# Optimization experiments

Measured on AMD Instinct MI355X. Metric: run time of the kernel, lower is better.

The kernel has to match this reference:

```python
import itertools
import jax, jax.numpy as jnp
import numpy as np

N, C, D, S = 512, 128, 16, 10  # atoms, channels, irreps dim (0e+1o+2e+3o), species
IR_DIMS = {'0e': 1, '1o': 3}
MULS = {'0e': (23, 4, 1), '1o': (33, 6, 1)}  # path multiplicities for orders (3, 2, 1)


def _make_u(key, order, mul, ir_dim):
    # Synthetic stand-in for e3nn.reduced_symmetric_tensor_product_basis:
    # under permutation of the `order` leading D axes.
    shape = (D,) * order + (mul, ir_dim)
    u = jax.random.normal(key, shape, dtype=jnp.float32)
    mask = jax.random.bernoulli(jax.random.fold_in(key, 1), 0.1, shape)
    u = jnp.where(mask, u, 0.0)
    perms = list(itertools.permutations(range(order)))
    u = sum(jnp.transpose(u, p + (order, order + 1)) for p in perms) / len(perms)
    return u


def setup_inputs() -> dict:
    key = jax.random.key(0)
    ks = jax.random.split(key, 16)
    inp = {
        'x': jax.random.normal(ks[0], (N, C, D), dtype=jnp.float32),
        'index': jax.random.randint(ks[1], (N,), 0, S, dtype=jnp.int32),
    }
    i = 2
    for ir in IR_DIMS:
        for order, mul in zip((3, 2, 1), MULS[ir]):
            inp[f'u{order}_{ir}'] = _make_u(ks[i], order, mul, IR_DIMS[ir]); i += 1
            # gradient_normalization='element' -> init stddev mul**-0.5, no runtime scale
            inp[f'w{order}_{ir}'] = (jax.random.normal(ks[i], (S, mul, C), dtype=jnp.float32)
                                     * mul ** -0.5); i += 1
    return inp


def _contract(x, idx, u3, u2, u1, w3, w2, w1):
    # x: (N,C,D); uK: (D,)*K + (mulK, ir); wK: (S, mulK, C)
    w3i, w2i, w1i = w3[idx], w2[idx], w1[idx]  # species gather -> (N, mulK, C)
    # order 3: einsum('...jki,kc,cj->c...i', u3, w3i, x) batched over atoms.
    # Form p[n,c,k,j] = w3i[n,k,c]*x[n,c,j] first (small), then one big contraction.
    p = jnp.einsum('nkc,ncj->nckj', w3i, x)              # (N,C,mul3,D)
    out = jnp.einsum('abjki,nckj->ncabi', u3, p)         # (N,C,D,D,ir)
    # order 2: accumulate U2.w2, then contract one D axis with x
    out = out + jnp.einsum('abki,nkc->ncabi', u2, w2i)   # (N,C,D,D,ir)
    out = jnp.einsum('ncaji,ncj->ncai', out, x)          # (N,C,D,ir)
    # order 1: accumulate U1.w1, then final contraction with x
    out = out + jnp.einsum('aki,nkc->ncai', u1, w1i)     # (N,C,D,ir)
    out = jnp.einsum('ncji,ncj->nci', out, x)            # (N,C,ir)
    return out


def reference(x, index, u3_0e, w3_0e, u2_0e, w2_0e, u1_0e, w1_0e,
              u3_1o, w3_1o, u2_1o, w2_1o, u1_1o, w1_1o):
    out0 = _contract(x, index, u3_0e, u2_0e, u1_0e, w3_0e, w2_0e, w1_0e)  # (N,C,1)
    out1 = _contract(x, index, u3_1o, u2_1o, u1_1o, w3_1o, w2_1o, w1_1o)  # (N,C,3)
    return jnp.concatenate([out0, out1], axis=-1)  # (N,C,4) irreps 0e+1o
```

## Files before the change

### kernel.cpp

```cpp
#include <hip/hip_runtime.h>
#include <hip/hip_fp16.h>


#define DD     16
#define NATOM  512
#define NCH    128
#define NSPEC  10
#define NTP    1024
#define ATB    4
#define APT    1
#define MAXB   136
#define CHUNKS 8
#define NTC    128
#define TILE   8
#define NTILES (NTC / TILE)
#define CHALF  2
#define CT     8

#define WS_DESC  0
#define WS_ORDER 1024
#define WS_COEF  8192
#define COEF_BYTES (NSPEC * 2 * NTP * 64 * 4 * 2)
#define WS_PART  (WS_COEF + COEF_BYTES)

struct TermTable { unsigned v[NTP]; };
constexpr TermTable build_terms() {
  TermTable T{};
  int t = 0;
  for (int a = 0; a < DD; a++)
    for (int b = a; b < DD; b++)
      for (int j = b; j < DD; j++) {
        unsigned m = (a == b && b == j) ? 1u : ((a == b || b == j) ? 3u : 6u);
        T.v[t++] = (unsigned)(a | (b << 5) | (j << 10) | (3u << 15) | (m << 18));
      }
  for (int a = 0; a < DD; a++)
    for (int b = a; b < DD; b++) {
      unsigned m = (a == b) ? 1u : 2u;
      T.v[t++] = (unsigned)(a | (b << 5) | (16 << 10) | (2u << 15) | (m << 18));
    }
  for (int a = 0; a < DD; a++)
    T.v[t++] = (unsigned)(a | (16 << 5) | (16 << 10) | (1u << 15) | (1u << 18));
  while (t < NTP) T.v[t++] = (unsigned)(17 | (17 << 5) | (17 << 10));
  return T;
}
constexpr TermTable TERMS = build_terms();

__device__ void do_setup(const int* __restrict__ index, int* __restrict__ desc,
                         int* __restrict__ order) {
  __shared__ int cnt[NSPEC], cursor[NSPEC], bbase[NSPEC + 1];
  const int tid = threadIdx.x;
  if (tid < NSPEC) { cnt[tid] = 0; cursor[tid] = 0; }
  __syncthreads();
  for (int i = tid; i < NATOM; i += 128) atomicAdd(&cnt[index[i]], 1);
  for (int i = tid; i < MAXB * ATB; i += 128) order[i] = -1;
  __syncthreads();
  if (tid == 0) {
    int base = 0;
    for (int s = 0; s < NSPEC; s++) { bbase[s] = base; base += (cnt[s] + ATB - 1) / ATB; }
    bbase[NSPEC] = base;
  }
  __syncthreads();
  for (int i = tid; i < NATOM; i += 128) {
    int s = index[i];
    int pos = atomicAdd(&cursor[s], 1);
    order[bbase[s] * ATB + pos] = i;
  }
  for (int i = tid; i < MAXB; i += 128) {
    int sp = -1;
    for (int s = 0; s < NSPEC; s++)
      if (i >= bbase[s] && i < bbase[s + 1]) sp = s;
    desc[i] = sp;
  }
}

__global__ __launch_bounds__(128) void coef_setup_kernel(
    const float* __restrict__ u3_0, const float* __restrict__ w3_0,
    const float* __restrict__ u2_0, const float* __restrict__ w2_0,
    const float* __restrict__ u1_0, const float* __restrict__ w1_0,
    const float* __restrict__ u3_1, const float* __restrict__ w3_1,
    const float* __restrict__ u2_1, const float* __restrict__ w2_1,
    const float* __restrict__ u1_1, const float* __restrict__ w1_1,
    const int* __restrict__ index, int* __restrict__ desc,
    int* __restrict__ order, __half* __restrict__ coefh) {
  if (blockIdx.y == NTP / CT) {
    if (blockIdx.x == 0) do_setup(index, desc, order);
    return;
  }
  const int s = blockIdx.x;
  const int c = threadIdx.x;
  const int tbase = blockIdx.y * CT;

  __shared__ float us0[CT][23];
  __shared__ float us1[CT][99];

  for (int i = 0; i < CT; ++i) {
    const unsigned ev = TERMS.v[tbase + i];
    const int kind = (ev >> 15) & 7;
    const int a = ev & 31, b = (ev >> 5) & 31, j = (ev >> 10) & 31;
    if (kind == 3) {
      const int off = (a * DD + b) * DD + j;
      if (c < 23) us0[i][c] = u3_0[off * 23 + c];
      else if (c < 122) us1[i][c - 23] = u3_1[(size_t)off * 99 + (c - 23)];
    } else if (kind == 2) {
      const int off = a * DD + b;
      if (c < 4) us0[i][c] = u2_0[off * 4 + c];
      else if (c < 22) us1[i][c - 4] = u2_1[off * 18 + (c - 4)];
    } else if (kind == 1) {
      if (c < 1) us0[i][0] = u1_0[a];
      else if (c < 4) us1[i][c - 1] = u1_1[a * 3 + (c - 1)];
    }
  }
  __syncthreads();

  float r3_0[23], r3_1[33], r2_0[4], r2_1[6];
#pragma unroll
  for (int k = 0; k < 23; k++) r3_0[k] = w3_0[(s * 23 + k) * NCH + c];
#pragma unroll
  for (int k = 0; k < 33; k++) r3_1[k] = w3_1[(s * 33 + k) * NCH + c];
#pragma unroll
  for (int k = 0; k < 4; k++) r2_0[k] = w2_0[(s * 4 + k) * NCH + c];
#pragma unroll
  for (int k = 0; k < 6; k++) r2_1[k] = w2_1[(s * 6 + k) * NCH + c];
  const float r1_0 = w1_0[s * NCH + c];
  const float r1_1 = w1_1[s * NCH + c];

  for (int i = 0; i < CT; ++i) {
    const unsigned ev = TERMS.v[tbase + i];
    const int kind = (ev >> 15) & 7;
    const float fm = (float)((ev >> 18) & 7);
    float s0 = 0.f, s1 = 0.f, s2 = 0.f, s3 = 0.f;
    if (kind == 3) {
#pragma unroll
      for (int k = 0; k < 23; k++) s0 += us0[i][k] * r3_0[k];
#pragma unroll
      for (int k = 0; k < 33; k++) {
        const float w = r3_1[k];
        s1 += us1[i][k * 3 + 0] * w;
        s2 += us1[i][k * 3 + 1] * w;
        s3 += us1[i][k * 3 + 2] * w;
      }
    } else if (kind == 2) {
#pragma unroll
      for (int k = 0; k < 4; k++) s0 += us0[i][k] * r2_0[k];
#pragma unroll
      for (int k = 0; k < 6; k++) {
        const float w = r2_1[k];
        s1 += us1[i][k * 3 + 0] * w;
        s2 += us1[i][k * 3 + 1] * w;
        s3 += us1[i][k * 3 + 2] * w;
      }
    } else if (kind == 1) {
      s0 = us0[i][0] * r1_0;
      s1 = us1[i][0] * r1_1;
      s2 = us1[i][1] * r1_1;
      s3 = us1[i][2] * r1_1;
    }
    union { __half2 h2[2]; uint2 u; } pk;
    pk.h2[0] = __floats2half2_rn(fm * s0, fm * s1);
    pk.h2[1] = __floats2half2_rn(fm * s2, fm * s3);
    const size_t off =
        (((size_t)(s * 2 + (c >> 6)) * NTP + (tbase + i)) * 64 + (c & 63));
    *(uint2*)((char*)coefh + off * 8) = pk.u;
  }
}

__device__ __forceinline__ void stage_tile(const unsigned* __restrict__ gbase,
                                           int t0_tile, float* dst_base,
                                           int wave, int lane) {
  const unsigned* g = gbase + (size_t)(t0_tile + 2 * wave) * 128 + lane * 4;
  __builtin_amdgcn_global_load_lds(
      (const __attribute__((address_space(1))) unsigned int*)g,
      (__attribute__((address_space(3))) unsigned int*)(dst_base + wave * 256),
      16, 0, 0);
}

template <int CH>
__device__ __forceinline__ void eval_chunk(const unsigned* __restrict__ gbase,
                                           float (*lbuf)[TILE * 128],
                                           int wave, int lane,
                                           const float (&xr)[18],
                                           float (&ac)[4]) {
  constexpr int T0 = CH * NTC;
  stage_tile(gbase, T0, &lbuf[0][0], wave, lane);
#pragma unroll
  for (int tile = 0; tile < NTILES; ++tile) {
    __syncthreads();
    if (tile + 1 < NTILES)
      stage_tile(gbase, T0 + (tile + 1) * TILE, &lbuf[(tile + 1) & 1][0], wave, lane);
    const float* lb = &lbuf[tile & 1][0];
#pragma unroll
    for (int i = 0; i < TILE; ++i) {
      const unsigned ev = TERMS.v[T0 + tile * TILE + i];
      const int ea = ev & 31, eb = (ev >> 5) & 31, ej = (ev >> 10) & 31;
      const uint2 raw = *(const uint2*)(lb + i * 128 + lane * 2);
      const float2 f01 = __half22float2(*reinterpret_cast<const __half2*>(&raw.x));
      const float2 f23 = __half22float2(*reinterpret_cast<const __half2*>(&raw.y));
      const float m = xr[ea] * xr[eb] * xr[ej];
      ac[0] += f01.x * m; ac[1] += f01.y * m;
      ac[2] += f23.x * m; ac[3] += f23.y * m;
    }
  }
}

__device__ __forceinline__ void load16(float (&xr)[18], const float* __restrict__ p) {
  const float4* q = (const float4*)p;
  const float4 v0 = q[0], v1 = q[1], v2 = q[2], v3 = q[3];
  xr[0] = v0.x; xr[1] = v0.y; xr[2] = v0.z; xr[3] = v0.w;
  xr[4] = v1.x; xr[5] = v1.y; xr[6] = v1.z; xr[7] = v1.w;
  xr[8] = v2.x; xr[9] = v2.y; xr[10] = v2.z; xr[11] = v2.w;
  xr[12] = v3.x; xr[13] = v3.y; xr[14] = v3.z; xr[15] = v3.w;
}

__global__ __launch_bounds__(256, 4) void contract_kernel(const float* __restrict__ x,
                                                          const int* __restrict__ desc,
                                                          const int* __restrict__ order,
                                                          const __half* __restrict__ coefh,
                                                          float* __restrict__ partial) {
  const int s = desc[blockIdx.x];
  if (s < 0) return;
  const int lane = threadIdx.x & 63;
  const int wave = threadIdx.x >> 6;
  const int half = blockIdx.z;
  const int c = half * 64 + lane;

  __shared__ float lbuf[2][TILE * 128];

  const int n = order[blockIdx.x * ATB + wave];

  float xr[18];
#pragma unroll
  for (int i = 0; i < DD; i++) xr[i] = 0.f;
  xr[16] = 1.f;
  xr[17] = 0.f;
  if (n >= 0) load16(xr, x + ((size_t)n * NCH + c) * DD);

  float ac[4] = {0.f, 0.f, 0.f, 0.f};

  const unsigned* gbase =
      (const unsigned*)coefh + (size_t)(s * 2 + half) * NTP * 128;

  switch (blockIdx.y) {
    case 0: eval_chunk<0>(gbase, lbuf, wave, lane, xr, ac); break;
    case 1: eval_chunk<1>(gbase, lbuf, wave, lane, xr, ac); break;
    case 2: eval_chunk<2>(gbase, lbuf, wave, lane, xr, ac); break;
    case 3: eval_chunk<3>(gbase, lbuf, wave, lane, xr, ac); break;
    case 4: eval_chunk<4>(gbase, lbuf, wave, lane, xr, ac); break;
    case 5: eval_chunk<5>(gbase, lbuf, wave, lane, xr, ac); break;
    case 6: eval_chunk<6>(gbase, lbuf, wave, lane, xr, ac); break;
    default: eval_chunk<7>(gbase, lbuf, wave, lane, xr, ac); break;
  }

  if (n >= 0) {
    float* pb = partial + (size_t)blockIdx.y * (NATOM * NCH * 4);
    *(float4*)(pb + ((size_t)n * NCH + c) * 4) =
        float4{ac[0], ac[1], ac[2], ac[3]};
  }
}

__global__ __launch_bounds__(256) void reduce_kernel(const float4* __restrict__ partial,
                                                     float4* __restrict__ out) {
  const int i = blockIdx.x * 256 + threadIdx.x;
  float4 s{0.f, 0.f, 0.f, 0.f};
#pragma unroll
  for (int ch = 0; ch < CHUNKS; ch++) {
    const float4 v = partial[(size_t)ch * (NATOM * NCH) + i];
    s.x += v.x; s.y += v.y; s.z += v.z; s.w += v.w;
  }
  out[i] = s;
}

extern "C" void kernel_launch(void* const* d_in, const int* in_sizes, int n_in,
                              void* d_out, int out_size, void* d_ws, size_t ws_size,
                              hipStream_t stream) {
  const float* x    = (const float*)d_in[0];
  const int* index  = (const int*)d_in[1];
  const float* u3_0 = (const float*)d_in[2];
  const float* w3_0 = (const float*)d_in[3];
  const float* u2_0 = (const float*)d_in[4];
  const float* w2_0 = (const float*)d_in[5];
  const float* u1_0 = (const float*)d_in[6];
  const float* w1_0 = (const float*)d_in[7];
  const float* u3_1 = (const float*)d_in[8];
  const float* w3_1 = (const float*)d_in[9];
  const float* u2_1 = (const float*)d_in[10];
  const float* w2_1 = (const float*)d_in[11];
  const float* u1_1 = (const float*)d_in[12];
  const float* w1_1 = (const float*)d_in[13];
  float* out = (float*)d_out;

  char* ws = (char*)d_ws;
  int* desc      = (int*)(ws + WS_DESC);
  int* order     = (int*)(ws + WS_ORDER);
  __half* coefh  = (__half*)(ws + WS_COEF);
  float* partial = (float*)(ws + WS_PART);

  coef_setup_kernel<<<dim3(NSPEC, NTP / CT + 1), 128, 0, stream>>>(
      u3_0, w3_0, u2_0, w2_0, u1_0, w1_0,
      u3_1, w3_1, u2_1, w2_1, u1_1, w1_1, index, desc, order, coefh);
  contract_kernel<<<dim3(MAXB, CHUNKS, CHALF), 256, 0, stream>>>(x, desc, order, coefh, partial);
  reduce_kernel<<<(NATOM * NCH) / 256, 256, 0, stream>>>((const float4*)partial, (float4*)out);
}
```

Measured before the change: 129.8 us.

## Map atoms to lanes with wave-uniform coefficients and drop the chunked reduction

The contraction is restructured so each 64-thread block handles up to 64 atoms of one species for a single channel. The per-term coefficients are then identical across the wave and can be read directly from global memory as uniform loads, instead of being staged through LDS tiles. The coefficient layout becomes contiguous per (species, channel), and each thread loops over all 968 terms, writing its result straight to the output. This removes the partial-sum buffer, the separate reduce kernel and the LDS double-buffering. In exchange, the fully unrolled 968-term loop produces a very large kernel body, and x loads are strided across atoms.

```diff
diff --git a/kernel.cpp b/kernel.cpp
--- a/kernel.cpp
+++ b/kernel.cpp
@@ -7,21 +7,15 @@
 #define NCH    128
 #define NSPEC  10
 #define NTP    1024
-#define ATB    4
-#define APT    1
-#define MAXB   136
-#define CHUNKS 8
-#define NTC    128
-#define TILE   8
-#define NTILES (NTC / TILE)
-#define CHALF  2
+#define NT     968
+#define ATB    64
+#define MAXB   18
 #define CT     8
 
 #define WS_DESC  0
 #define WS_ORDER 1024
 #define WS_COEF  8192
-#define COEF_BYTES (NSPEC * 2 * NTP * 64 * 4 * 2)
-#define WS_PART  (WS_COEF + COEF_BYTES)
+#define COEF_BYTES (NSPEC * NCH * NTP * 4 * 2)
 
 struct TermTable { unsigned v[NTP]; };
 constexpr TermTable build_terms() {
@@ -124,6 +118,7 @@
   const float r1_0 = w1_0[s * NCH + c];
   const float r1_1 = w1_1[s * NCH + c];
 
+  uint2* outp = (uint2*)coefh + ((size_t)(s * NCH + c) * NTP + tbase);
   for (int i = 0; i < CT; ++i) {
     const unsigned ev = TERMS.v[tbase + i];
     const int kind = (ev >> 15) & 7;
@@ -158,47 +153,7 @@
     union { __half2 h2[2]; uint2 u; } pk;
     pk.h2[0] = __floats2half2_rn(fm * s0, fm * s1);
     pk.h2[1] = __floats2half2_rn(fm * s2, fm * s3);
-    const size_t off =
-        (((size_t)(s * 2 + (c >> 6)) * NTP + (tbase + i)) * 64 + (c & 63));
-    *(uint2*)((char*)coefh + off * 8) = pk.u;
-  }
-}
-
-__device__ __forceinline__ void stage_tile(const unsigned* __restrict__ gbase,
-                                           int t0_tile, float* dst_base,
-                                           int wave, int lane) {
-  const unsigned* g = gbase + (size_t)(t0_tile + 2 * wave) * 128 + lane * 4;
-  __builtin_amdgcn_global_load_lds(
-      (const __attribute__((address_space(1))) unsigned int*)g,
-      (__attribute__((address_space(3))) unsigned int*)(dst_base + wave * 256),
-      16, 0, 0);
-}
-
-template <int CH>
-__device__ __forceinline__ void eval_chunk(const unsigned* __restrict__ gbase,
-                                           float (*lbuf)[TILE * 128],
-                                           int wave, int lane,
-                                           const float (&xr)[18],
-                                           float (&ac)[4]) {
-  constexpr int T0 = CH * NTC;
-  stage_tile(gbase, T0, &lbuf[0][0], wave, lane);
-#pragma unroll
-  for (int tile = 0; tile < NTILES; ++tile) {
-    __syncthreads();
-    if (tile + 1 < NTILES)
-      stage_tile(gbase, T0 + (tile + 1) * TILE, &lbuf[(tile + 1) & 1][0], wave, lane);
-    const float* lb = &lbuf[tile & 1][0];
-#pragma unroll
-    for (int i = 0; i < TILE; ++i) {
-      const unsigned ev = TERMS.v[T0 + tile * TILE + i];
-      const int ea = ev & 31, eb = (ev >> 5) & 31, ej = (ev >> 10) & 31;
-      const uint2 raw = *(const uint2*)(lb + i * 128 + lane * 2);
-      const float2 f01 = __half22float2(*reinterpret_cast<const __half2*>(&raw.x));
-      const float2 f23 = __half22float2(*reinterpret_cast<const __half2*>(&raw.y));
-      const float m = xr[ea] * xr[eb] * xr[ej];
-      ac[0] += f01.x * m; ac[1] += f01.y * m;
-      ac[2] += f23.x * m; ac[3] += f23.y * m;
-    }
+    outp[i] = pk.u;
   }
 }
 
@@ -211,21 +166,17 @@
   xr[12] = v3.x; xr[13] = v3.y; xr[14] = v3.z; xr[15] = v3.w;
 }
 
-__global__ __launch_bounds__(256, 4) void contract_kernel(const float* __restrict__ x,
-                                                          const int* __restrict__ desc,
-                                                          const int* __restrict__ order,
-                                                          const __half* __restrict__ coefh,
-                                                          float* __restrict__ partial) {
-  const int s = desc[blockIdx.x];
+__global__ __launch_bounds__(64) void contract_kernel(const float* __restrict__ x,
+                                                      const int* __restrict__ desc,
+                                                      const int* __restrict__ order,
+                                                      const __half* __restrict__ coefh,
+                                                      float* __restrict__ out) {
+  const int b = blockIdx.x;
+  const int c = blockIdx.y;
+  const int s = desc[b];
   if (s < 0) return;
-  const int lane = threadIdx.x & 63;
-  const int wave = threadIdx.x >> 6;
-  const int half = blockIdx.z;
-  const int c = half * 64 + lane;
-
-  __shared__ float lbuf[2][TILE * 128];
-
-  const int n = order[blockIdx.x * ATB + wave];
+  const int lane = threadIdx.x;
+  const int n = order[b * ATB + lane];
 
   float xr[18];
 #pragma unroll
@@ -236,37 +187,23 @@
 
   float ac[4] = {0.f, 0.f, 0.f, 0.f};
 
-  const unsigned* gbase =
-      (const unsigned*)coefh + (size_t)(s * 2 + half) * NTP * 128;
-
-  switch (blockIdx.y) {
-    case 0: eval_chunk<0>(gbase, lbuf, wave, lane, xr, ac); break;
-    case 1: eval_chunk<1>(gbase, lbuf, wave, lane, xr, ac); break;
-    case 2: eval_chunk<2>(gbase, lbuf, wave, lane, xr, ac); break;
-    case 3: eval_chunk<3>(gbase, lbuf, wave, lane, xr, ac); break;
-    case 4: eval_chunk<4>(gbase, lbuf, wave, lane, xr, ac); break;
-    case 5: eval_chunk<5>(gbase, lbuf, wave, lane, xr, ac); break;
-    case 6: eval_chunk<6>(gbase, lbuf, wave, lane, xr, ac); break;
-    default: eval_chunk<7>(gbase, lbuf, wave, lane, xr, ac); break;
-  }
-
-  if (n >= 0) {
-    float* pb = partial + (size_t)blockIdx.y * (NATOM * NCH * 4);
-    *(float4*)(pb + ((size_t)n * NCH + c) * 4) =
+  const uint2* cc = (const uint2*)coefh + (size_t)(s * NCH + c) * NTP;
+
+#pragma unroll
+  for (int t = 0; t < NT; ++t) {
+    const unsigned ev = TERMS.v[t];
+    const int ea = ev & 31, eb = (ev >> 5) & 31, ej = (ev >> 10) & 31;
+    const uint2 raw = cc[t];
+    const float2 f01 = __half22float2(*reinterpret_cast<const __half2*>(&raw.x));
+    const float2 f23 = __half22float2(*reinterpret_cast<const __half2*>(&raw.y));
+    const float m = xr[ea] * xr[eb] * xr[ej];
+    ac[0] += f01.x * m; ac[1] += f01.y * m;
+    ac[2] += f23.x * m; ac[3] += f23.y * m;
+  }
+
+  if (n >= 0)
+    *(float4*)(out + ((size_t)n * NCH + c) * 4) =
         float4{ac[0], ac[1], ac[2], ac[3]};
-  }
-}
-
-__global__ __launch_bounds__(256) void reduce_kernel(const float4* __restrict__ partial,
-                                                     float4* __restrict__ out) {
-  const int i = blockIdx.x * 256 + threadIdx.x;
-  float4 s{0.f, 0.f, 0.f, 0.f};
-#pragma unroll
-  for (int ch = 0; ch < CHUNKS; ch++) {
-    const float4 v = partial[(size_t)ch * (NATOM * NCH) + i];
-    s.x += v.x; s.y += v.y; s.z += v.z; s.w += v.w;
-  }
-  out[i] = s;
 }
 
 extern "C" void kernel_launch(void* const* d_in, const int* in_sizes, int n_in,
@@ -292,11 +229,9 @@
   int* desc      = (int*)(ws + WS_DESC);
   int* order     = (int*)(ws + WS_ORDER);
   __half* coefh  = (__half*)(ws + WS_COEF);
-  float* partial = (float*)(ws + WS_PART);
 
   coef_setup_kernel<<<dim3(NSPEC, NTP / CT + 1), 128, 0, stream>>>(
       u3_0, w3_0, u2_0, w2_0, u1_0, w1_0,
       u3_1, w3_1, u2_1, w2_1, u1_1, w1_1, index, desc, order, coefh);
-  contract_kernel<<<dim3(MAXB, CHUNKS, CHALF), 256, 0, stream>>>(x, desc, order, coefh, partial);
-  reduce_kernel<<<(NATOM * NCH) / 256, 256, 0, stream>>>((const float4*)partial, (float4*)out);
-}
+  contract_kernel<<<dim3(MAXB, NCH), 64, 0, stream>>>(x, desc, order, coefh, out);
+}
```

New measurement: 199.9 us. 1.54x slower.
